# Optimization experiments

Hardware: AMD Instinct MI355X
Metric: run time of the kernel (lower is better)

The kernel has to match this reference:

```python
import jax, jax.numpy as jnp
import numpy as np

EMBED_DIM = 2048
HEAD_DIM = 128
B, T = 4, 2048


def setup_inputs() -> dict:
    key = jax.random.key(0)
    k1, k2, k3, k4 = jax.random.split(key, 4)
    x_in = jax.random.normal(k1, (B, T, EMBED_DIM), dtype=jnp.float32)
    scale = 1.0 / np.sqrt(EMBED_DIM)
    Wq = jax.random.normal(k2, (EMBED_DIM, HEAD_DIM), dtype=jnp.float32) * scale
    Wk = jax.random.normal(k3, (EMBED_DIM, HEAD_DIM), dtype=jnp.float32) * scale
    Wv = jax.random.normal(k4, (EMBED_DIM, HEAD_DIM), dtype=jnp.float32) * scale
    return {"x_in": x_in, "Wq": Wq, "Wk": Wk, "Wv": Wv}


def reference(x_in, Wq, Wk, Wv):
    # x_in: [B, T, E]; projections (Linear, no bias)
    q = jnp.einsum('bte,ed->btd', x_in, Wq)  # [B,T,D]
    k = jnp.einsum('bte,ed->btd', x_in, Wk)
    v = jnp.einsum('bte,ed->btd', x_in, Wv)
    t = x_in.shape[1]
    d = Wq.shape[1]
    s = jnp.einsum('btd,bsd->bts', q, k) / jnp.sqrt(jnp.asarray(d, q.dtype))  # [B,Tq,Tk]
    # causal mask: positions with tril==0 (k index > q index) -> -inf
    causal = jnp.tril(jnp.ones((t, t), dtype=bool))
    s = jnp.where(causal, s, -jnp.inf)
    # NOTE: original module applies softmax over dim=1 (query axis), faithfully reproduced
    a = jax.nn.softmax(s, axis=1)
    z = jnp.einsum('bts,bsd->btd', a, v)  # [B,T,D]
    return z
```

## Files before the change

### kernel.cpp

```cpp
#include <hip/hip_runtime.h>

typedef _Float16 f16x8 __attribute__((ext_vector_type(8)));
typedef _Float16 f16x4 __attribute__((ext_vector_type(4)));
typedef float f32x4 __attribute__((ext_vector_type(4)));

#define T_DIM 2048
#define E_DIM 2048
#define D_DIM 128
#define NB 4
#define KSP_P 4
#define KCH_P 512
#define KSP_A 8
#define KCH_A 256
#define NCH2 32

__device__ __forceinline__ void gll16(const void* g, void* l) {
  __builtin_amdgcn_global_load_lds(
      (const __attribute__((address_space(1))) unsigned int*)g,
      (__attribute__((address_space(3))) unsigned int*)l, 16, 0, 0);
}

__device__ __forceinline__ void merge_stat(float& m, float& l, float pm, float pl) {
  if (pm != -__builtin_inff()) {
    float nm = fmaxf(m, pm);
    l = l * __expf(m - nm) + pl * __expf(pm - nm);
    m = nm;
  }
}


__global__ void cvt_w(const float* __restrict__ Wq, const float* __restrict__ Wk,
                      const float* __restrict__ Wv, _Float16* __restrict__ WhT) {
  int idx = blockIdx.x * 256 + threadIdx.x;
  int w = blockIdx.y;
  const float* W = (w == 0) ? Wq : ((w == 1) ? Wk : Wv);
  int e = idx & (E_DIM - 1), d = idx >> 11;
  WhT[(size_t)w * (D_DIM * E_DIM) + idx] = (_Float16)W[e * D_DIM + d];
}


__global__ __launch_bounds__(768) void proj_gemm(
    const float* __restrict__ x, const _Float16* __restrict__ WhT,
    _Float16* __restrict__ Ph) {
  __shared__ float Asw[2][128 * 32];
  __shared__ _Float16 Bsw[2][384 * 32];
  const int tid = threadIdx.x, w = tid >> 6, lane = tid & 63;
  const int wn = w >> 1, wr = w & 1, quad = lane >> 4, l16 = lane & 15;
  const int t0 = blockIdx.x * 128;
  const int ks = blockIdx.y;
  const int kb = ks * KCH_P;
  const int ar = tid >> 3, aseg = tid & 7;
  const int br = tid >> 2, bseg = tid & 3;

  auto stage = [&](int buf, int k0) {
    {
      int g = aseg ^ (ar & 7);
      gll16(x + (size_t)(t0 + ar) * E_DIM + k0 + g * 4, &Asw[buf][ar * 32 + aseg * 4]);
      if (tid < 256) {
        int r = 96 + ar;
        int g2 = aseg ^ (r & 7);
        gll16(x + (size_t)(t0 + r) * E_DIM + k0 + g2 * 4, &Asw[buf][r * 32 + aseg * 4]);
      }
    }
    {
      int g = bseg ^ ((br >> 1) & 3);
      gll16(WhT + (size_t)br * E_DIM + k0 + g * 8, &Bsw[buf][br * 32 + bseg * 8]);
      int r = 192 + br;
      int g2 = bseg ^ ((r >> 1) & 3);
      gll16(WhT + (size_t)r * E_DIM + k0 + g2 * 8, &Bsw[buf][r * 32 + bseg * 8]);
    }
  };

  f32x4 acc[4][4] = {};
  stage(0, kb);
  const int NIT = KCH_P / 32;
  for (int it = 0; it < NIT; ++it) {
    const int cur = it & 1;
    asm volatile("s_waitcnt vmcnt(0)" ::: "memory");
    __syncthreads();
    if (it + 1 < NIT) stage(cur ^ 1, kb + (it + 1) * 32);
    f16x8 af[4], bf[4];
#pragma unroll
    for (int i = 0; i < 4; ++i) {
      int row = wr * 64 + i * 16 + l16;
      int s0 = (2 * quad) ^ (row & 7);
      int s1 = (2 * quad + 1) ^ (row & 7);
      f32x4 a0 = *(const f32x4*)(&Asw[cur][row * 32 + s0 * 4]);
      f32x4 a1 = *(const f32x4*)(&Asw[cur][row * 32 + s1 * 4]);
#pragma unroll
      for (int e = 0; e < 4; ++e) {
        af[i][e] = (_Float16)a0[e];
        af[i][e + 4] = (_Float16)a1[e];
      }
    }
#pragma unroll
    for (int j = 0; j < 4; ++j) {
      int row = wn * 64 + j * 16 + l16;
      int sg = quad ^ ((row >> 1) & 3);
      bf[j] = *(const f16x8*)(&Bsw[cur][row * 32 + sg * 8]);
    }
#pragma unroll
    for (int i = 0; i < 4; ++i)
#pragma unroll
      for (int j = 0; j < 4; ++j)
        acc[i][j] = __builtin_amdgcn_mfma_f32_16x16x32_f16(af[i], bf[j], acc[i][j], 0, 0, 0);
  }
  const int mat = wn >> 1;
  const int nb0 = (wn & 1) * 64;
  _Float16* P = Ph + ((size_t)(ks * 3 + mat) << 20);
  if (mat < 2) {
#pragma unroll
    for (int i = 0; i < 4; ++i)
#pragma unroll
      for (int j = 0; j < 4; ++j) {
        int n = nb0 + j * 16 + l16;
#pragma unroll
        for (int r = 0; r < 4; ++r) {
          int t = t0 + wr * 64 + i * 16 + quad * 4 + r;
          P[(size_t)t * D_DIM + n] = (_Float16)acc[i][j][r];
        }
      }
  } else {
#pragma unroll
    for (int i = 0; i < 4; ++i)
#pragma unroll
      for (int j = 0; j < 4; ++j) {
        int n = nb0 + j * 16 + l16;
        int t = t0 + wr * 64 + i * 16 + quad * 4;
        f16x4 o;
#pragma unroll
        for (int r = 0; r < 4; ++r) o[r] = (_Float16)acc[i][j][r];
        *(f16x4*)(P + ((size_t)(t >> 11) * D_DIM + n) * T_DIM + (t & (T_DIM - 1))) = o;
      }
  }
}


__global__ void proj_reduce(const _Float16* __restrict__ Ph, _Float16* __restrict__ Qh,
                            _Float16* __restrict__ Kh, _Float16* __restrict__ VT) {
  size_t u = ((size_t)blockIdx.x * 256 + threadIdx.x) * 8;
  int mat = (int)(u >> 20);
  size_t rem = u & ((1u << 20) - 1);
  float s[8] = {};
#pragma unroll
  for (int ks = 0; ks < KSP_P; ++ks) {
    f16x8 p = *(const f16x8*)(Ph + ((size_t)(ks * 3 + mat) << 20) + rem);
#pragma unroll
    for (int e = 0; e < 8; ++e) s[e] += (float)p[e];
  }
  f16x8 o;
#pragma unroll
  for (int e = 0; e < 8; ++e) o[e] = (_Float16)s[e];
  _Float16* dst = (mat == 0) ? Qh : ((mat == 1) ? Kh : VT);
  *(f16x8*)(dst + rem) = o;
}


__global__ __launch_bounds__(256) void s_gemm(const _Float16* __restrict__ Qh,
                                              const _Float16* __restrict__ Kh,
                                              _Float16* __restrict__ S,
                                              float* __restrict__ Pm,
                                              float* __restrict__ Pl) {
  int idx = blockIdx.x;
  int xt = (int)((sqrtf(8.f * idx + 1.f) - 1.f) * 0.5f);
  while ((xt + 1) * (xt + 2) / 2 <= idx) ++xt;
  while (xt * (xt + 1) / 2 > idx) --xt;
  int yt = idx - xt * (xt + 1) / 2;
  __shared__ _Float16 Bs[4][128 * 32];
  const int tid = threadIdx.x, w = tid >> 6, lane = tid & 63;
  const int wr = w >> 1, wc = w & 1, quad = lane >> 4, l16 = lane & 15;
  const int t0 = xt * 128, s0 = yt * 128, b = blockIdx.y;
  const _Float16* A = Qh + (size_t)b * T_DIM * D_DIM;
  const _Float16* B = Kh + (size_t)b * T_DIM * D_DIM;
  const int srow = lane >> 2;
  const int swz = ((lane & 3) ^ ((srow >> 1) & 3)) * 8;
#pragma unroll
  for (int kq = 0; kq < 4; ++kq)
#pragma unroll
    for (int q = 0; q < 2; ++q) {
      int rbase = w * 32 + q * 16;
      gll16(B + (size_t)(s0 + rbase + srow) * D_DIM + kq * 32 + swz,
            Bs[kq] + rbase * 32);
    }
  __syncthreads();
  f32x4 acc[4][4] = {};
  const int bsg = (quad ^ ((l16 >> 1) & 3)) * 8;
#pragma unroll
  for (int kq = 0; kq < 4; ++kq) {
    f16x8 af[4], bf[4];
#pragma unroll
    for (int i = 0; i < 4; ++i)
      af[i] = *(const f16x8*)(A + (size_t)(t0 + wr * 64 + i * 16 + l16) * D_DIM +
                              kq * 32 + quad * 8);
#pragma unroll
    for (int j = 0; j < 4; ++j)
      bf[j] = *(const f16x8*)(Bs[kq] + (wc * 64 + j * 16 + l16) * 32 + bsg);
#pragma unroll
    for (int i = 0; i < 4; ++i)
#pragma unroll
      for (int j = 0; j < 4; ++j)
        acc[i][j] = __builtin_amdgcn_mfma_f32_16x16x32_f16(af[i], bf[j], acc[i][j], 0, 0, 0);
  }
  _Float16* Sb = S + (size_t)b * T_DIM * T_DIM;
  const float scale = 0.08838834764831845f;
  const float NEG = -__builtin_inff();
#pragma unroll
  for (int j = 0; j < 4; ++j) {
    const int s = s0 + wc * 64 + j * 16 + l16;
    float m = NEG;
#pragma unroll
    for (int i = 0; i < 4; ++i)
#pragma unroll
      for (int r = 0; r < 4; ++r) {
        int t = t0 + wr * 64 + i * 16 + quad * 4 + r;
        float v = (s > t) ? NEG : acc[i][j][r] * scale;
        Sb[(size_t)t * T_DIM + s] = (_Float16)v;
        m = fmaxf(m, v);
      }
    float l = 0.f;
    if (m != NEG) {
#pragma unroll
      for (int i = 0; i < 4; ++i)
#pragma unroll
        for (int r = 0; r < 4; ++r) {
          int t = t0 + wr * 64 + i * 16 + quad * 4 + r;
          float v = (s > t) ? NEG : acc[i][j][r] * scale;
          l += __expf(v - m);
        }
    }
#pragma unroll
    for (int d = 16; d <= 32; d <<= 1) {
      float pm = __shfl_xor(m, d, 64);
      float pl = __shfl_xor(l, d, 64);
      merge_stat(m, l, pm, pl);
    }
    if (quad == 0) {
      int c = 2 * xt + wr;
      Pm[((size_t)c * NB + b) * T_DIM + s] = m;
      Pl[((size_t)c * NB + b) * T_DIM + s] = l;
    }
  }
}


__global__ __launch_bounds__(256) void comb_stats(const float* __restrict__ Pm,
                                                  const float* __restrict__ Pl,
                                                  float* __restrict__ M,
                                                  float* __restrict__ L) {
  __shared__ float sM[8][32];
  __shared__ float sL[8][32];
  const int g = threadIdx.x >> 5, sl = threadIdx.x & 31;
  const int c = blockIdx.x * 32 + sl;
  const int b = c >> 11, s = c & (T_DIM - 1);
  float m = -__builtin_inff(), l = 0.f;
#pragma unroll
  for (int k = 0; k < NCH2 / 8; ++k) {
    int ch = g * (NCH2 / 8) + k;
    if (ch >= (s >> 6)) {
      size_t idx = ((size_t)ch * NB + b) * T_DIM + s;
      merge_stat(m, l, Pm[idx], Pl[idx]);
    }
  }
  sM[g][sl] = m;
  sL[g][sl] = l;
  __syncthreads();
  if (threadIdx.x < 32) {
    const int c2 = blockIdx.x * 32 + threadIdx.x;
    float fm = -__builtin_inff(), fl = 0.f;
#pragma unroll
    for (int gg = 0; gg < 8; ++gg) merge_stat(fm, fl, sM[gg][threadIdx.x], sL[gg][threadIdx.x]);
    M[c2] = fm;
    L[c2] = 1.f / fl;
  }
}


__global__ __launch_bounds__(256) void av_gemm(const _Float16* __restrict__ S,
                                               const _Float16* __restrict__ VT,
                                               const float* __restrict__ M,
                                               const float* __restrict__ L,
                                               float* __restrict__ Zp) {
  const int t0 = blockIdx.x * 128, b = blockIdx.y, ks = blockIdx.z;
  const int Kmax = t0 + 128;
  const int Kstart = ks * KCH_A;
  if (Kstart >= Kmax) return;
  const int Kend = (Kstart + KCH_A < Kmax) ? (Kstart + KCH_A) : Kmax;
  __shared__ _Float16 As[128 * 32];
  __shared__ _Float16 Bs[128 * 32];
  __shared__ float Ms[KCH_A];
  __shared__ float Ls[KCH_A];
  const int tid = threadIdx.x, w = tid >> 6, lane = tid & 63;
  const int wr = w >> 1, wc = w & 1, quad = lane >> 4, l16 = lane & 15;
  const _Float16* Sb = S + (size_t)b * T_DIM * T_DIM;
  const _Float16* Vb = VT + (size_t)b * D_DIM * T_DIM;
  for (int i = tid; i < Kend - Kstart; i += 256) {
    Ms[i] = M[b * T_DIM + Kstart + i];
    Ls[i] = L[b * T_DIM + Kstart + i];
  }
  const int srow = lane >> 2, scol = (lane & 3) * 8;
  f32x4 acc[4][4] = {};
  for (int k0 = Kstart; k0 < Kend; k0 += 32) {
    __syncthreads();
#pragma unroll
    for (int q = 0; q < 2; ++q) {
      int u = q * 256 + tid;
      int row = u >> 2, c8 = (u & 3) * 8;
      int sc = k0 + c8;
      f16x8 v = *(const f16x8*)(Sb + (size_t)(t0 + row) * T_DIM + sc);
      f16x8 o;
#pragma unroll
      for (int e = 0; e < 8; ++e) {
        int li = sc + e - Kstart;
        float a = __expf((float)v[e] - Ms[li]) * Ls[li];
        o[e] = (_Float16)a;
      }
      *(f16x8*)(As + row * 32 + c8) = o;
      int rbase = w * 32 + q * 16;
      gll16(Vb + (size_t)(rbase + srow) * T_DIM + k0 + scol, Bs + rbase * 32);
    }
    __syncthreads();
    f16x8 af[4], bf[4];
#pragma unroll
    for (int i = 0; i < 4; ++i)
      af[i] = *(const f16x8*)(As + (wr * 64 + i * 16 + l16) * 32 + quad * 8);
#pragma unroll
    for (int j = 0; j < 4; ++j)
      bf[j] = *(const f16x8*)(Bs + (wc * 64 + j * 16 + l16) * 32 + quad * 8);
#pragma unroll
    for (int i = 0; i < 4; ++i)
#pragma unroll
      for (int j = 0; j < 4; ++j)
        acc[i][j] = __builtin_amdgcn_mfma_f32_16x16x32_f16(af[i], bf[j], acc[i][j], 0, 0, 0);
  }
  float* Zb = Zp + ((size_t)ks * NB + b) * T_DIM * D_DIM;
#pragma unroll
  for (int i = 0; i < 4; ++i)
#pragma unroll
    for (int j = 0; j < 4; ++j) {
      int n = wc * 64 + j * 16 + l16;
#pragma unroll
      for (int r = 0; r < 4; ++r) {
        int t = t0 + wr * 64 + i * 16 + quad * 4 + r;
        Zb[(size_t)t * D_DIM + n] = acc[i][j][r];
      }
    }
}


__global__ void z_reduce(const float* __restrict__ Zp, float* __restrict__ Z) {
  size_t flat = ((size_t)blockIdx.x * 256 + threadIdx.x) * 4;
  int t = (int)((flat >> 7) & (T_DIM - 1));
  int ns = ((t >> 7) + 2) >> 1;
  f32x4 s = {};
  for (int ks = 0; ks < ns; ++ks) {
    f32x4 p = *(const f32x4*)(Zp + ((size_t)ks * NB * T_DIM * D_DIM) + flat);
    s += p;
  }
  *(f32x4*)(Z + flat) = s;
}


extern "C" void kernel_launch(void* const* d_in, const int* in_sizes, int n_in,
                              void* d_out, int out_size, void* d_ws, size_t ws_size,
                              hipStream_t stream) {
  const float* x = (const float*)d_in[0];
  const float* Wq = (const float*)d_in[1];
  const float* Wk = (const float*)d_in[2];
  const float* Wv = (const float*)d_in[3];
  char* ws = (char*)d_ws;
  float* Zp = (float*)(ws);
  _Float16* WhT = (_Float16*)(ws + 33554432);
  _Float16* Qh = (_Float16*)(ws + 35127296);
  _Float16* Kh = (_Float16*)(ws + 37224448);
  _Float16* VT = (_Float16*)(ws + 39321600);
  _Float16* S = (_Float16*)(ws + 41418752);
  _Float16* Ph = (_Float16*)(ws + 41418752);
  float* M = (float*)(ws + 74973184);
  float* L = (float*)(ws + 75005952);
  float* Pm = (float*)(ws + 75038720);
  float* Pl = (float*)(ws + 76087296);
  float* Z = (float*)d_out;

  cvt_w<<<dim3(1024, 3), 256, 0, stream>>>(Wq, Wk, Wv, WhT);
  proj_gemm<<<dim3(64, KSP_P), 768, 0, stream>>>(x, WhT, Ph);
  proj_reduce<<<1536, 256, 0, stream>>>(Ph, Qh, Kh, VT);
  s_gemm<<<dim3(136, 4), 256, 0, stream>>>(Qh, Kh, S, Pm, Pl);
  comb_stats<<<256, 256, 0, stream>>>(Pm, Pl, M, L);
  av_gemm<<<dim3(16, 4, KSP_A), 256, 0, stream>>>(S, VT, M, L, Zp);
  z_reduce<<<1024, 256, 0, stream>>>(Zp, Z);
}
```

Measured before the change: 170.3 us.

## Double-buffer A operands through registers and convert to fp16 before LDS

In proj_gemm, x tiles are now loaded into registers, converted to fp16 and written to LDS after the MFMA block, replacing fp32 LDS staging with per-read conversion. This halves A's LDS footprint and removes repeated conversions, but it drops the XOR swizzle on A, so LDS bank conflicts may rise. av_gemm gets the same register-prefetch double buffer for the exp-normalised S tile and V, letting global loads overlap the MFMAs, and both kernels raise wave priority around the MFMA block. The score-stats loop now caches the masked scores instead of recomputing them.

```diff
diff --git a/kernel.cpp b/kernel.cpp
--- a/kernel.cpp
+++ b/kernel.cpp
@@ -42,56 +42,61 @@
 __global__ __launch_bounds__(768) void proj_gemm(
     const float* __restrict__ x, const _Float16* __restrict__ WhT,
     _Float16* __restrict__ Ph) {
-  __shared__ float Asw[2][128 * 32];
+  __shared__ _Float16 A16[2][128 * 32];
   __shared__ _Float16 Bsw[2][384 * 32];
   const int tid = threadIdx.x, w = tid >> 6, lane = tid & 63;
   const int wn = w >> 1, wr = w & 1, quad = lane >> 4, l16 = lane & 15;
   const int t0 = blockIdx.x * 128;
   const int ks = blockIdx.y;
   const int kb = ks * KCH_P;
-  const int ar = tid >> 3, aseg = tid & 7;
+  const int arowA = tid >> 2, asegA = tid & 3;
   const int br = tid >> 2, bseg = tid & 3;
 
-  auto stage = [&](int buf, int k0) {
-    {
-      int g = aseg ^ (ar & 7);
-      gll16(x + (size_t)(t0 + ar) * E_DIM + k0 + g * 4, &Asw[buf][ar * 32 + aseg * 4]);
-      if (tid < 256) {
-        int r = 96 + ar;
-        int g2 = aseg ^ (r & 7);
-        gll16(x + (size_t)(t0 + r) * E_DIM + k0 + g2 * 4, &Asw[buf][r * 32 + aseg * 4]);
-      }
-    }
-    {
-      int g = bseg ^ ((br >> 1) & 3);
-      gll16(WhT + (size_t)br * E_DIM + k0 + g * 8, &Bsw[buf][br * 32 + bseg * 8]);
-      int r = 192 + br;
-      int g2 = bseg ^ ((r >> 1) & 3);
-      gll16(WhT + (size_t)r * E_DIM + k0 + g2 * 8, &Bsw[buf][r * 32 + bseg * 8]);
-    }
+  f32x4 ax0, ax1;
+  auto loadA = [&](int k0) {
+    if (tid < 512) {
+      const float* src = x + (size_t)(t0 + arowA) * E_DIM + k0 + asegA * 8;
+      ax0 = *(const f32x4*)src;
+      ax1 = *(const f32x4*)(src + 4);
+    }
+  };
+  auto writeA = [&](int buf) {
+    if (tid < 512) {
+      f16x8 o;
+#pragma unroll
+      for (int e = 0; e < 4; ++e) {
+        o[e] = (_Float16)ax0[e];
+        o[e + 4] = (_Float16)ax1[e];
+      }
+      *(f16x8*)(&A16[buf][arowA * 32 + asegA * 8]) = o;
+    }
+  };
+  auto stageB = [&](int buf, int k0) {
+    int g = bseg ^ ((br >> 1) & 3);
+    gll16(WhT + (size_t)br * E_DIM + k0 + g * 8, &Bsw[buf][br * 32 + bseg * 8]);
+    int r = 192 + br;
+    int g2 = bseg ^ ((r >> 1) & 3);
+    gll16(WhT + (size_t)r * E_DIM + k0 + g2 * 8, &Bsw[buf][r * 32 + bseg * 8]);
   };
 
   f32x4 acc[4][4] = {};
-  stage(0, kb);
+  loadA(kb);
+  stageB(0, kb);
+  asm volatile("s_waitcnt vmcnt(0)" ::: "memory");
+  writeA(0);
   const int NIT = KCH_P / 32;
   for (int it = 0; it < NIT; ++it) {
     const int cur = it & 1;
-    asm volatile("s_waitcnt vmcnt(0)" ::: "memory");
     __syncthreads();
-    if (it + 1 < NIT) stage(cur ^ 1, kb + (it + 1) * 32);
+    if (it + 1 < NIT) {
+      loadA(kb + (it + 1) * 32);
+      stageB(cur ^ 1, kb + (it + 1) * 32);
+    }
     f16x8 af[4], bf[4];
 #pragma unroll
     for (int i = 0; i < 4; ++i) {
       int row = wr * 64 + i * 16 + l16;
-      int s0 = (2 * quad) ^ (row & 7);
-      int s1 = (2 * quad + 1) ^ (row & 7);
-      f32x4 a0 = *(const f32x4*)(&Asw[cur][row * 32 + s0 * 4]);
-      f32x4 a1 = *(const f32x4*)(&Asw[cur][row * 32 + s1 * 4]);
-#pragma unroll
-      for (int e = 0; e < 4; ++e) {
-        af[i][e] = (_Float16)a0[e];
-        af[i][e + 4] = (_Float16)a1[e];
-      }
+      af[i] = *(const f16x8*)(&A16[cur][row * 32 + quad * 8]);
     }
 #pragma unroll
     for (int j = 0; j < 4; ++j) {
@@ -99,11 +104,17 @@
       int sg = quad ^ ((row >> 1) & 3);
       bf[j] = *(const f16x8*)(&Bsw[cur][row * 32 + sg * 8]);
     }
+    __builtin_amdgcn_s_setprio(1);
 #pragma unroll
     for (int i = 0; i < 4; ++i)
 #pragma unroll
       for (int j = 0; j < 4; ++j)
         acc[i][j] = __builtin_amdgcn_mfma_f32_16x16x32_f16(af[i], bf[j], acc[i][j], 0, 0, 0);
+    __builtin_amdgcn_s_setprio(0);
+    if (it + 1 < NIT) {
+      asm volatile("s_waitcnt vmcnt(0)" ::: "memory");
+      writeA(cur ^ 1);
+    }
   }
   const int mat = wn >> 1;
   const int nb0 = (wn & 1) * 64;
@@ -207,6 +218,7 @@
 #pragma unroll
   for (int j = 0; j < 4; ++j) {
     const int s = s0 + wc * 64 + j * 16 + l16;
+    float vv[16];
     float m = NEG;
 #pragma unroll
     for (int i = 0; i < 4; ++i)
@@ -215,18 +227,13 @@
         int t = t0 + wr * 64 + i * 16 + quad * 4 + r;
         float v = (s > t) ? NEG : acc[i][j][r] * scale;
         Sb[(size_t)t * T_DIM + s] = (_Float16)v;
+        vv[i * 4 + r] = v;
         m = fmaxf(m, v);
       }
     float l = 0.f;
     if (m != NEG) {
 #pragma unroll
-      for (int i = 0; i < 4; ++i)
-#pragma unroll
-        for (int r = 0; r < 4; ++r) {
-          int t = t0 + wr * 64 + i * 16 + quad * 4 + r;
-          float v = (s > t) ? NEG : acc[i][j][r] * scale;
-          l += __expf(v - m);
-        }
+      for (int k = 0; k < 16; ++k) l += __expf(vv[k] - m);
     }
 #pragma unroll
     for (int d = 16; d <= 32; d <<= 1) {
@@ -285,8 +292,9 @@
   const int Kstart = ks * KCH_A;
   if (Kstart >= Kmax) return;
   const int Kend = (Kstart + KCH_A < Kmax) ? (Kstart + KCH_A) : Kmax;
-  __shared__ _Float16 As[128 * 32];
-  __shared__ _Float16 Bs[128 * 32];
+  const int nit = (Kend - Kstart) >> 5;
+  __shared__ _Float16 As[2][128 * 32];
+  __shared__ _Float16 Bs[2][128 * 32];
   __shared__ float Ms[KCH_A];
   __shared__ float Ls[KCH_A];
   const int tid = threadIdx.x, w = tid >> 6, lane = tid & 63;
@@ -298,39 +306,64 @@
     Ls[i] = L[b * T_DIM + Kstart + i];
   }
   const int srow = lane >> 2, scol = (lane & 3) * 8;
+  const int arow = tid >> 2, ac8 = (tid & 3) * 8;
+  f16x8 sv0, sv1;
+  auto loadS = [&](int k0) {
+    sv0 = *(const f16x8*)(Sb + (size_t)(t0 + arow) * T_DIM + k0 + ac8);
+    sv1 = *(const f16x8*)(Sb + (size_t)(t0 + 64 + arow) * T_DIM + k0 + ac8);
+  };
+  auto stageB = [&](int buf, int k0) {
+#pragma unroll
+    for (int q = 0; q < 2; ++q) {
+      int rbase = w * 32 + q * 16;
+      gll16(Vb + (size_t)(rbase + srow) * T_DIM + k0 + scol, Bs[buf] + rbase * 32);
+    }
+  };
+  auto writeA = [&](int buf, int k0) {
+#pragma unroll
+    for (int q = 0; q < 2; ++q) {
+      f16x8 v = q ? sv1 : sv0;
+      f16x8 o;
+#pragma unroll
+      for (int e = 0; e < 8; ++e) {
+        int li = k0 + ac8 + e - Kstart;
+        o[e] = (_Float16)(__expf((float)v[e] - Ms[li]) * Ls[li]);
+      }
+      *(f16x8*)(As[buf] + (q * 64 + arow) * 32 + ac8) = o;
+    }
+  };
   f32x4 acc[4][4] = {};
-  for (int k0 = Kstart; k0 < Kend; k0 += 32) {
+  __syncthreads();
+  loadS(Kstart);
+  stageB(0, Kstart);
+  asm volatile("s_waitcnt vmcnt(0)" ::: "memory");
+  writeA(0, Kstart);
+  for (int it = 0; it < nit; ++it) {
+    const int cur = it & 1;
+    const int k0 = Kstart + it * 32;
     __syncthreads();
-#pragma unroll
-    for (int q = 0; q < 2; ++q) {
-      int u = q * 256 + tid;
-      int row = u >> 2, c8 = (u & 3) * 8;
-      int sc = k0 + c8;
-      f16x8 v = *(const f16x8*)(Sb + (size_t)(t0 + row) * T_DIM + sc);
-      f16x8 o;
-#pragma unroll
-      for (int e = 0; e < 8; ++e) {
-        int li = sc + e - Kstart;
-        float a = __expf((float)v[e] - Ms[li]) * Ls[li];
-        o[e] = (_Float16)a;
-      }
-      *(f16x8*)(As + row * 32 + c8) = o;
-      int rbase = w * 32 + q * 16;
-      gll16(Vb + (size_t)(rbase + srow) * T_DIM + k0 + scol, Bs + rbase * 32);
-    }
-    __syncthreads();
+    if (it + 1 < nit) {
+      loadS(k0 + 32);
+      stageB(cur ^ 1, k0 + 32);
+    }
     f16x8 af[4], bf[4];
 #pragma unroll
     for (int i = 0; i < 4; ++i)
-      af[i] = *(const f16x8*)(As + (wr * 64 + i * 16 + l16) * 32 + quad * 8);
+      af[i] = *(const f16x8*)(As[cur] + (wr * 64 + i * 16 + l16) * 32 + quad * 8);
 #pragma unroll
     for (int j = 0; j < 4; ++j)
-      bf[j] = *(const f16x8*)(Bs + (wc * 64 + j * 16 + l16) * 32 + quad * 8);
+      bf[j] = *(const f16x8*)(Bs[cur] + (wc * 64 + j * 16 + l16) * 32 + quad * 8);
+    __builtin_amdgcn_s_setprio(1);
 #pragma unroll
     for (int i = 0; i < 4; ++i)
 #pragma unroll
       for (int j = 0; j < 4; ++j)
         acc[i][j] = __builtin_amdgcn_mfma_f32_16x16x32_f16(af[i], bf[j], acc[i][j], 0, 0, 0);
+    __builtin_amdgcn_s_setprio(0);
+    if (it + 1 < nit) {
+      asm volatile("s_waitcnt vmcnt(0)" ::: "memory");
+      writeA(cur ^ 1, k0 + 32);
+    }
   }
   float* Zb = Zp + ((size_t)ks * NB + b) * T_DIM * D_DIM;
 #pragma unroll
```

New measurement: 166.5 us. -2.2%, faster.
